# Kernel optimization log

Measured on AMD Instinct MI355X. Metric: run time of the kernel, lower is better.

## Reference

```python
import jax, jax.numpy as jnp
from jax import lax
import numpy as np

BIG = jnp.float32(1e6)  # 'no feature in this column' sentinel distance


def setup_inputs() -> dict:
    key = jax.random.key(0)
    k1, k2 = jax.random.split(key)
    # Binary segmentation masks in {0,1}; surf() only uses astype(bool), i.e. != 0.
    pred = (jax.random.uniform(k1, (512, 512)) > 0.5).astype(jnp.float32)
    gt = (jax.random.uniform(k2, (512, 512)) > 0.5).astype(jnp.float32)
    return {"pred": pred, "gt": gt}


def _erode(x):
    # scipy binary_erosion with connectivity-1 (cross) structure, border_value=0:
    # pixel survives iff it and its 4 neighbors are all True (out-of-bounds = False).
    p = jnp.pad(x, 1, constant_values=False)
    return x & p[:-2, 1:-1] & p[2:, 1:-1] & p[1:-1, :-2] & p[1:-1, 2:]


def _edt(feat):
    # Exact Euclidean distance from every pixel to the nearest True pixel of `feat`.
    # Equals scipy distance_transform_edt(~feat) in the original code.
    H, W = feat.shape
    # --- pass 1: per-column 1D distance |r - k| to nearest feature (two sweeps) ---
    def sweep(carry, row):
        c = jnp.where(row, jnp.float32(0.0), carry + jnp.float32(1.0))
        return c, c
    init = jnp.full((W,), BIG, dtype=jnp.float32)
    _, df = lax.scan(sweep, init, feat)          # distance to nearest feature above
    _, db = lax.scan(sweep, init, feat[::-1])    # ... below
    g = jnp.minimum(df, db[::-1])                # [H, W] vertical distance
    g2 = g * g
    # --- pass 2: row-wise min-plus over column offsets (exact, separable) ---
    j = jnp.arange(W, dtype=jnp.float32)
    delta2 = (j[:, None] - j[None, :]) ** 2      # [W(c), W(j)]
    # D[r, c] = min_j ( g2[r, j] + (c - j)^2 )   -> [H, W, W] intermediate
    d2 = jnp.min(g2[:, None, :] + delta2[None, :, :], axis=-1)
    return jnp.sqrt(d2)


def reference(pred, gt):
    p = pred != 0
    g = gt != 0
    # Surface = mask minus its erosion
    S = p & ~_erode(p)
    Sprime = g & ~_erode(g)
    dta = _edt(S)       # distance field to pred surface (== edt(~S))
    dtb = _edt(Sprime)  # distance field to gt surface
    sm = S.astype(jnp.float32)
    spm = Sprime.astype(jnp.float32)
    # mean of concat(dta[Sprime], dtb[S]) without dynamic shapes
    num = jnp.sum(dta * spm) + jnp.sum(dtb * sm)
    den = jnp.sum(spm) + jnp.sum(sm)
    return num / den
```

## Files before the change

kernel.cpp:

```cpp
#include <hip/hip_runtime.h>

#define HH 512
#define WW 512
#define NPIX (HH*WW)

__global__ __launch_bounds__(256) void surf_kernel(
        const float* __restrict__ pred, const float* __restrict__ gt,
        unsigned char* __restrict__ mA, unsigned char* __restrict__ mB,
        unsigned int* __restrict__ ticket) {
    int idx4 = blockIdx.x * 256 + threadIdx.x;
    if (idx4 == 0) { *ticket = 0u; }
    if (idx4 >= NPIX / 4) return;
    int r  = idx4 >> 7;
    int c4 = (idx4 & 127) << 2;

    const float* srcs[2] = { pred, gt };
    unsigned char* dsts[2] = { mA, mB };
    #pragma unroll
    for (int f = 0; f < 2; ++f) {
        const float* x = srcs[f];
        float4 v = ((const float4*)x)[idx4];
        float4 u = (r > 0)      ? ((const float4*)x)[idx4 - 128] : make_float4(0,0,0,0);
        float4 d = (r < HH - 1) ? ((const float4*)x)[idx4 + 128] : make_float4(0,0,0,0);
        float lS = (c4 > 0)        ? x[r * WW + c4 - 1] : 0.0f;
        float rS = (c4 + 4 < WW)   ? x[r * WW + c4 + 4] : 0.0f;
        float vv[4] = { v.x, v.y, v.z, v.w };
        float uu[4] = { u.x, u.y, u.z, u.w };
        float dd[4] = { d.x, d.y, d.z, d.w };
        uchar4 out;
        unsigned char* o = (unsigned char*)&out;
        #pragma unroll
        for (int e = 0; e < 4; ++e) {
            int c = c4 + e;
            bool ctr = vv[e] != 0.0f;
            bool up  = (r > 0)      && (uu[e] != 0.0f);
            bool dn  = (r < HH - 1) && (dd[e] != 0.0f);
            bool lf  = (c > 0)      && ((e == 0 ? lS : vv[e - 1]) != 0.0f);
            bool rt  = (c < WW - 1) && ((e == 3 ? rS : vv[e + 1]) != 0.0f);
            o[e] = (ctr && !(up && dn && lf && rt)) ? 1 : 0;
        }
        ((uchar4*)dsts[f])[idx4] = out;
    }
}

__global__ __launch_bounds__(512) void edt_kernel(
        const unsigned char* __restrict__ mA, const unsigned char* __restrict__ mB,
        double* __restrict__ partials, unsigned int* __restrict__ ticket,
        float* __restrict__ out) {
    __shared__ float sga[WW];
    __shared__ float sgb[WW];
    __shared__ double lred[16];
    __shared__ int winner;
    int r = blockIdx.x;
    int c = threadIdx.x;

    bool fa = mA[r * WW + c] != 0;
    bool fb = mB[r * WW + c] != 0;

    int foundA = fa ? 0 : -1;
    int foundB = fb ? 0 : -1;
    for (int k = 1; k < HH && (foundA < 0 || foundB < 0); ++k) {
        bool up = (r - k) >= 0, dn = (r + k) < HH;
        if (foundA < 0) {
            bool hit = (up && mA[(r - k) * WW + c] != 0) ||
                       (dn && mA[(r + k) * WW + c] != 0);
            if (hit) foundA = k;
        }
        if (foundB < 0) {
            bool hit = (up && mB[(r - k) * WW + c] != 0) ||
                       (dn && mB[(r + k) * WW + c] != 0);
            if (hit) foundB = k;
        }
    }
    float sent = 1e6f + (float)((r + 1 < HH - r) ? (r + 1) : (HH - r));
    float ga = (foundA >= 0) ? (float)foundA : sent;
    float gb = (foundB >= 0) ? (float)foundB : sent;
    sga[c] = ga * ga;
    sgb[c] = gb * gb;
    __syncthreads();

    float besta = sga[c];
    float bestb = sgb[c];
    for (int k = 1; k < WW; ++k) {
        float k2 = (float)(k * k);
        if (k2 >= besta && k2 >= bestb) break;
        int cl = c - k, cr = c + k;
        if (cl >= 0) {
            besta = fminf(besta, sga[cl] + k2);
            bestb = fminf(bestb, sgb[cl] + k2);
        }
        if (cr < WW) {
            besta = fminf(besta, sga[cr] + k2);
            bestb = fminf(bestb, sgb[cr] + k2);
        }
    }

    float wA = fa ? 1.0f : 0.0f;
    float wB = fb ? 1.0f : 0.0f;
    double lnum = (double)(sqrtf(besta) * wB + sqrtf(bestb) * wA);
    double lden = (double)(wA + wB);
    for (int off = 32; off > 0; off >>= 1) {
        lnum += __shfl_down(lnum, off, 64);
        lden += __shfl_down(lden, off, 64);
    }
    int wv = c >> 6;
    if ((c & 63) == 0) { lred[wv] = lnum; lred[8 + wv] = lden; }
    __syncthreads();
    if (c == 0) {
        double n = 0.0, d = 0.0;
        #pragma unroll
        for (int i = 0; i < 8; ++i) { n += lred[i]; d += lred[8 + i]; }
        partials[2 * r]     = n;
        partials[2 * r + 1] = d;
        __threadfence();
        unsigned int old = atomicAdd(ticket, 1u);
        winner = (old == HH - 1) ? 1 : 0;
    }
    __syncthreads();

    if (winner) {
        __threadfence();
        double n = partials[2 * c];
        double d = partials[2 * c + 1];
        for (int off = 32; off > 0; off >>= 1) {
            n += __shfl_down(n, off, 64);
            d += __shfl_down(d, off, 64);
        }
        if ((c & 63) == 0) { lred[c >> 6] = n; lred[8 + (c >> 6)] = d; }
        __syncthreads();
        if (c == 0) {
            double nn = 0.0, dd = 0.0;
            #pragma unroll
            for (int i = 0; i < 8; ++i) { nn += lred[i]; dd += lred[8 + i]; }
            out[0] = (float)(nn / dd);
        }
    }
}

extern "C" void kernel_launch(void* const* d_in, const int* in_sizes, int n_in,
                              void* d_out, int out_size, void* d_ws, size_t ws_size,
                              hipStream_t stream) {
    const float* pred = (const float*)d_in[0];
    const float* gt   = (const float*)d_in[1];
    float* out = (float*)d_out;

    char* ws = (char*)d_ws;
    unsigned int* tick = (unsigned int*)ws;
    double* partials   = (double*)(ws + 256);
    unsigned char* mA  = (unsigned char*)(ws + 256 + 8192);
    unsigned char* mB  = mA + NPIX;

    surf_kernel<<<NPIX / 4 / 256, 256, 0, stream>>>(pred, gt, mA, mB, tick);
    edt_kernel<<<HH, 512, 0, stream>>>(mA, mB, partials, tick, out);
}
```

Before: 75.63 us.

## Pack both surface masks into one byte array and unroll EDT search loops

Stores the pred and gt surface masks as two bits of a single byte array, so the vertical search reads one byte per row for both masks and the global mask traffic is halved. The column search now loads four rows at a time, which raises memory-level parallelism at the cost of some loads past the first hit. The row min-plus pass reads an interleaved float2 from shared memory and is unrolled by four with the early-exit check done once per block of four offsets, which may evaluate a few extra offsets.

```diff
diff --git a/kernel.cpp b/kernel.cpp
--- a/kernel.cpp
+++ b/kernel.cpp
@@ -6,16 +6,15 @@
 
 __global__ __launch_bounds__(256) void surf_kernel(
         const float* __restrict__ pred, const float* __restrict__ gt,
-        unsigned char* __restrict__ mA, unsigned char* __restrict__ mB,
-        unsigned int* __restrict__ ticket) {
+        unsigned char* __restrict__ mAB, unsigned int* __restrict__ ticket) {
     int idx4 = blockIdx.x * 256 + threadIdx.x;
     if (idx4 == 0) { *ticket = 0u; }
     if (idx4 >= NPIX / 4) return;
     int r  = idx4 >> 7;
     int c4 = (idx4 & 127) << 2;
 
+    unsigned char bits[4] = {0, 0, 0, 0};
     const float* srcs[2] = { pred, gt };
-    unsigned char* dsts[2] = { mA, mB };
     #pragma unroll
     for (int f = 0; f < 2; ++f) {
         const float* x = srcs[f];
@@ -27,8 +26,6 @@
         float vv[4] = { v.x, v.y, v.z, v.w };
         float uu[4] = { u.x, u.y, u.z, u.w };
         float dd[4] = { d.x, d.y, d.z, d.w };
-        uchar4 out;
-        unsigned char* o = (unsigned char*)&out;
         #pragma unroll
         for (int e = 0; e < 4; ++e) {
             int c = c4 + e;
@@ -37,61 +34,72 @@
             bool dn  = (r < HH - 1) && (dd[e] != 0.0f);
             bool lf  = (c > 0)      && ((e == 0 ? lS : vv[e - 1]) != 0.0f);
             bool rt  = (c < WW - 1) && ((e == 3 ? rS : vv[e + 1]) != 0.0f);
-            o[e] = (ctr && !(up && dn && lf && rt)) ? 1 : 0;
+            if (ctr && !(up && dn && lf && rt)) bits[e] |= (1 << f);
         }
-        ((uchar4*)dsts[f])[idx4] = out;
     }
+    uchar4 out;
+    out.x = bits[0]; out.y = bits[1]; out.z = bits[2]; out.w = bits[3];
+    ((uchar4*)mAB)[idx4] = out;
 }
 
 __global__ __launch_bounds__(512) void edt_kernel(
-        const unsigned char* __restrict__ mA, const unsigned char* __restrict__ mB,
+        const unsigned char* __restrict__ mAB,
         double* __restrict__ partials, unsigned int* __restrict__ ticket,
         float* __restrict__ out) {
-    __shared__ float sga[WW];
-    __shared__ float sgb[WW];
+    __shared__ float2 s2[WW];
     __shared__ double lred[16];
     __shared__ int winner;
     int r = blockIdx.x;
     int c = threadIdx.x;
 
-    bool fa = mA[r * WW + c] != 0;
-    bool fb = mB[r * WW + c] != 0;
+    unsigned int own = mAB[r * WW + c];
+    bool fa = (own & 1u) != 0u;
+    bool fb = (own & 2u) != 0u;
 
     int foundA = fa ? 0 : -1;
     int foundB = fb ? 0 : -1;
-    for (int k = 1; k < HH && (foundA < 0 || foundB < 0); ++k) {
-        bool up = (r - k) >= 0, dn = (r + k) < HH;
-        if (foundA < 0) {
-            bool hit = (up && mA[(r - k) * WW + c] != 0) ||
-                       (dn && mA[(r + k) * WW + c] != 0);
-            if (hit) foundA = k;
+    for (int kb = 1; kb < HH && (foundA < 0 || foundB < 0); kb += 4) {
+        unsigned int mu[4], md[4];
+        #pragma unroll
+        for (int i = 0; i < 4; ++i) {
+            int ku = kb + i;
+            int ru = r - ku, rd = r + ku;
+            mu[i] = (ru >= 0) ? (unsigned int)mAB[ru * WW + c] : 0u;
+            md[i] = (rd < HH) ? (unsigned int)mAB[rd * WW + c] : 0u;
         }
-        if (foundB < 0) {
-            bool hit = (up && mB[(r - k) * WW + c] != 0) ||
-                       (dn && mB[(r + k) * WW + c] != 0);
-            if (hit) foundB = k;
+        #pragma unroll
+        for (int i = 0; i < 4; ++i) {
+            unsigned int hit = mu[i] | md[i];
+            if (foundA < 0 && (hit & 1u)) foundA = kb + i;
+            if (foundB < 0 && (hit & 2u)) foundB = kb + i;
         }
     }
     float sent = 1e6f + (float)((r + 1 < HH - r) ? (r + 1) : (HH - r));
     float ga = (foundA >= 0) ? (float)foundA : sent;
     float gb = (foundB >= 0) ? (float)foundB : sent;
-    sga[c] = ga * ga;
-    sgb[c] = gb * gb;
+    s2[c] = make_float2(ga * ga, gb * gb);
     __syncthreads();
 
-    float besta = sga[c];
-    float bestb = sgb[c];
-    for (int k = 1; k < WW; ++k) {
-        float k2 = (float)(k * k);
-        if (k2 >= besta && k2 >= bestb) break;
-        int cl = c - k, cr = c + k;
-        if (cl >= 0) {
-            besta = fminf(besta, sga[cl] + k2);
-            bestb = fminf(bestb, sgb[cl] + k2);
-        }
-        if (cr < WW) {
-            besta = fminf(besta, sga[cr] + k2);
-            bestb = fminf(bestb, sgb[cr] + k2);
+    float2 o2 = s2[c];
+    float besta = o2.x, bestb = o2.y;
+    for (int kb = 1; kb < WW; kb += 4) {
+        float kk2 = (float)(kb * kb);
+        if (kk2 >= besta && kk2 >= bestb) break;
+        #pragma unroll
+        for (int i = 0; i < 4; ++i) {
+            int k = kb + i;
+            float k2 = (float)(k * k);
+            int cl = c - k, cr = c + k;
+            if (cl >= 0) {
+                float2 g = s2[cl];
+                besta = fminf(besta, g.x + k2);
+                bestb = fminf(bestb, g.y + k2);
+            }
+            if (cr < WW) {
+                float2 g = s2[cr];
+                besta = fminf(besta, g.x + k2);
+                bestb = fminf(bestb, g.y + k2);
+            }
         }
     }
 
@@ -147,9 +155,8 @@
     char* ws = (char*)d_ws;
     unsigned int* tick = (unsigned int*)ws;
     double* partials   = (double*)(ws + 256);
-    unsigned char* mA  = (unsigned char*)(ws + 256 + 8192);
-    unsigned char* mB  = mA + NPIX;
+    unsigned char* mAB = (unsigned char*)(ws + 256 + 8192);
 
-    surf_kernel<<<NPIX / 4 / 256, 256, 0, stream>>>(pred, gt, mA, mB, tick);
-    edt_kernel<<<HH, 512, 0, stream>>>(mA, mB, partials, tick, out);
+    surf_kernel<<<NPIX / 4 / 256, 256, 0, stream>>>(pred, gt, mAB, tick);
+    edt_kernel<<<HH, 512, 0, stream>>>(mAB, partials, tick, out);
 }
```

Result: faster. 72.90 us (median of 2 runs) (-3.6%).
